# Performance work log

Measured on AMD Instinct MI355X. Metric: run time of the kernel, lower is better.

Reference implementation:

```python
import jax, jax.numpy as jnp
import numpy as np

EPS = 1e-6
DECAY = 0.9   # spike_decay
THR = 0.5     # spike_threshold
SBETA = 10.0  # surrogate beta
KW = 4        # depthwise short-conv kernel width (causal)


def _rms(x, w):
    return x * jax.lax.rsqrt(jnp.mean(x * x, axis=-1, keepdims=True) + EPS) * w


def setup_inputs() -> dict:
    B, T, D, H, dk, dv, r, dff = 2, 2048, 1024, 8, 64, 64, 64, 4096
    keys = iter(jax.random.split(jax.random.key(0), 24))
    def g(shape, s=0.02):
        return jax.random.normal(next(keys), shape, jnp.float32) * s
    return {
        'x': jax.random.normal(next(keys), (B, T, D), jnp.float32),
        'norm_in_w': jnp.ones((D,), jnp.float32),
        'conv_w': g((D, 1, KW), 0.3),
        'conv_b': jnp.zeros((D,), jnp.float32),
        'Wq': g((D, H * dk)),
        'Wk': g((D, H * dk)),
        'Wv': g((D, H * dv)),
        'Wo': g((H * dv, D)),
        'Wspike': g((D, H * dk), 0.1),  # larger init so LIF actually spikes
        'Wau': g((D, r)),
        'bau': jnp.zeros((r,), jnp.float32),
        'Wad': g((r, H * dk)),
        'bad': jnp.zeros((H * dk,), jnp.float32),
        'alpha_spike': jnp.zeros((1, H, dk), jnp.float32),
        'Wbeta': g((D, H)),
        'bbeta': jnp.zeros((H,), jnp.float32),
        'beta_spike': jnp.zeros((1, H, dk), jnp.float32),
        'head_norm_w': jnp.ones((H, dv), jnp.float32),
        'Wu1': g((D, r)),
        'bu1': jnp.zeros((r,), jnp.float32),
        'Wu2': g((r, D)),
        'bu2': jnp.zeros((D,), jnp.float32),
        'ff_norm_w': jnp.ones((D,), jnp.float32),
        'Wff1': g((D, dff)),
        'Wff3': g((D, dff)),
        'Wff2': g((dff, D)),
    }


def reference(x, norm_in_w, conv_w, conv_b, Wq, Wk, Wv, Wo, Wspike,
              Wau, bau, Wad, bad, alpha_spike, Wbeta, bbeta, beta_spike,
              head_norm_w, Wu1, bu1, Wu2, bu2, ff_norm_w, Wff1, Wff3, Wff2):
    B, T, D = x.shape
    H, dk = alpha_spike.shape[1], alpha_spike.shape[2]
    dv = head_norm_w.shape[1]

    # --- input norm + causal depthwise short conv + SiLU ---
    h = _rms(x, norm_in_w)
    hc = jnp.transpose(h, (0, 2, 1))                         # [B,D,T]
    conv = jax.lax.conv_general_dilated(
        hc, conv_w, window_strides=(1,), padding=[(KW - 1, 0)],
        dimension_numbers=('NCH', 'OIH', 'NCH'), feature_group_count=D)
    conv = conv + conv_b[None, :, None]
    h = jax.nn.silu(jnp.transpose(conv, (0, 2, 1)))          # [B,T,D]

    def heads(z, d):
        return z.reshape(B, T, H, d)

    q = heads(h @ Wq, dk)
    k = heads(h @ Wk, dk)
    v = heads(h @ Wv, dv)
    q = q / (jnp.linalg.norm(q, axis=-1, keepdims=True) + 1e-6)
    k = k / (jnp.linalg.norm(k, axis=-1, keepdims=True) + 1e-6)
    drive = heads(h @ Wspike, dk)                            # LIF drive [B,T,H,dk]
    alpha_base = heads(jax.nn.silu(h @ Wau + bau) @ Wad + bad, dk)
    beta_base = h @ Wbeta + bbeta                            # [B,T,H]

    asp = alpha_spike[0]                                     # [H,dk]
    bsp = beta_spike[0]                                      # [H,dk]

    def step(carry, ins):
        s, mem = carry                                       # s [B,H,dk,dv], mem [B,H,dk]
        qt, kt, vt, dt, at, bt = ins
        # LIF with surrogate-gradient spike (straight-through), soft reset
        mem = DECAY * mem + dt
        sg = jax.nn.sigmoid(SBETA * (mem - THR))
        hard = (mem > THR).astype(mem.dtype)
        spike = sg + jax.lax.stop_gradient(hard - sg)
        mem = mem - spike * THR
        # spiking-modulated gates
        alpha = jax.nn.sigmoid(at + asp * spike)             # [B,H,dk]
        beta = jax.nn.sigmoid(bt[..., None] + jnp.sum(spike * bsp, -1, keepdims=True))  # [B,H,1]
        active = (jnp.sum(jnp.abs(spike), -1, keepdims=True) > 0).astype(qt.dtype)      # [B,H,1]
        alpha = jnp.where(active > 0, alpha, jnp.ones_like(alpha))
        beta = beta * active
        # gated delta-rule fast-weight update
        s = s * alpha[..., None]
        pred = jnp.einsum('bhk,bhkv->bhv', kt, s)
        s = s + (beta * kt)[..., None] * (vt - pred)[:, :, None, :]
        out = jnp.einsum('bhk,bhkv->bhv', qt, s)
        return (s, mem), out

    s0 = jnp.zeros((B, H, dk, dv), x.dtype)
    m0 = jnp.zeros((B, H, dk), x.dtype)
    xs = (jnp.moveaxis(q, 1, 0), jnp.moveaxis(k, 1, 0), jnp.moveaxis(v, 1, 0),
          jnp.moveaxis(drive, 1, 0), jnp.moveaxis(alpha_base, 1, 0),
          jnp.moveaxis(beta_base, 1, 0))
    _, y = jax.lax.scan(step, (s0, m0), xs)                  # [T,B,H,dv]
    y = jnp.moveaxis(y, 0, 1)                                # [B,T,H,dv]

    # headwise RMS norm, merge heads
    y = y * jax.lax.rsqrt(jnp.mean(y * y, axis=-1, keepdims=True) + EPS) * head_norm_w
    y = y.reshape(B, T, H * dv)

    # gated output projection + residual
    gate = jax.nn.sigmoid(jax.nn.silu(x @ Wu1 + bu1) @ Wu2 + bu2)
    y = x + (y @ Wo) * gate

    # SwiGLU FFN + residual
    z = _rms(y, ff_norm_w)
    y = y + (jax.nn.silu(z @ Wff1) * (z @ Wff3)) @ Wff2
    return y
```

## Files before the change

kernel.cpp:

```cpp
#include <hip/hip_runtime.h>
#include <hip/hip_bf16.h>

#define BB 2
#define TT 2048
#define DD 1024
#define HH 8
#define HKk 512
#define BTt 4096
#define CC 16
#define NT 128
#define PREPSZ 4608

typedef unsigned short u16;
typedef __attribute__((ext_vector_type(8))) short bf16x8;
typedef __attribute__((ext_vector_type(4))) float f32x4;

__device__ __forceinline__ u16 f2bf(float v) {
  union { float f; unsigned u; } c; c.f = v;
  return (u16)((c.u + 0x7fffu + ((c.u >> 16) & 1u)) >> 16);
}
__device__ __forceinline__ float bf2f(u16 v) {
  union { unsigned u; float f; } c; c.u = ((unsigned)v) << 16; return c.f;
}
__device__ __forceinline__ float sigm(float x) { return 1.f / (1.f + expf(-x)); }

__device__ __forceinline__ void gld16(const u16* g, u16* l) {
  __builtin_amdgcn_global_load_lds((const __attribute__((address_space(1))) void*)g,
                                   (__attribute__((address_space(3))) void*)l, 16, 0, 0);
}

struct TransJobs {
  const float* src[8];
  u16* dst[8];
  int K[8], N[8], rs[8], ro[8], lognx[8];
  int off[8];
};
__global__ __launch_bounds__(256) void ktransB(TransJobs J) {
  __shared__ u16 t[32][33];
  int bid = blockIdx.x;
  int j = 0;
#pragma unroll
  for (int q = 1; q < 8; q++) j += (bid >= J.off[q]) ? 1 : 0;
  int local = bid - J.off[j];
  const float* src = J.src[j];
  u16* dst = J.dst[j];
  int K = J.K[j], N = J.N[j], rs = J.rs[j], ro = J.ro[j];
  int nxm = (1 << J.lognx[j]) - 1;
  int n0 = (local & nxm) * 32, k0 = (local >> J.lognx[j]) * 32;
  int tx = threadIdx.x & 31, ty0 = threadIdx.x >> 5;
#pragma unroll
  for (int i = 0; i < 32; i += 8)
    t[ty0 + i][tx] = f2bf(src[(size_t)(k0 + ty0 + i) * N + n0 + tx]);
  __syncthreads();
#pragma unroll
  for (int i = 0; i < 32; i += 8)
    dst[((size_t)(n0 + ty0 + i) * rs + ro) * K + k0 + tx] = t[tx][ty0 + i];
}

__global__ __launch_bounds__(256) void krms(const float* __restrict__ x,
                                            const float* __restrict__ w,
                                            void* __restrict__ out, int obf) {
  size_t row = blockIdx.x;
  __shared__ float red[4];
  float vals[4];
  float s = 0.f;
#pragma unroll
  for (int i = 0; i < 4; i++) {
    vals[i] = x[row * DD + threadIdx.x + i * 256];
    s += vals[i] * vals[i];
  }
#pragma unroll
  for (int off = 32; off; off >>= 1) s += __shfl_xor(s, off);
  if ((threadIdx.x & 63) == 0) red[threadIdx.x >> 6] = s;
  __syncthreads();
  float tot = red[0] + red[1] + red[2] + red[3];
  float sc = rsqrtf(tot * (1.f / DD) + 1e-6f);
#pragma unroll
  for (int i = 0; i < 4; i++) {
    size_t idx = row * DD + threadIdx.x + i * 256;
    float vv = vals[i] * sc * w[threadIdx.x + i * 256];
    if (obf) ((u16*)out)[idx] = f2bf(vv);
    else ((float*)out)[idx] = vv;
  }
}

__global__ __launch_bounds__(256) void kconv(const float* __restrict__ hin,
                                             const float* __restrict__ cw,
                                             const float* __restrict__ cb,
                                             u16* __restrict__ hout) {
  size_t i = (size_t)blockIdx.x * 256 + threadIdx.x;
  int d = (int)(i & 1023);
  int bt = (int)(i >> 10);
  int b = bt >> 11, t = bt & 2047;
  float acc = cb[d];
#pragma unroll
  for (int j = 0; j < 4; j++) {
    int tt = t - 3 + j;
    if (tt >= 0) acc += hin[(((size_t)(b * TT + tt)) << 10) + d] * cw[d * 4 + j];
  }
  hout[i] = f2bf(acc * sigm(acc));
}

__global__ __launch_bounds__(256) void kgemm(const void* __restrict__ A, int abf,
                                             const float* __restrict__ Bm,
                                             const float* __restrict__ bias,
                                             float* __restrict__ C,
                                             int M, int N, int K, int act) {
  __shared__ __align__(16) float As[16][64];
  __shared__ __align__(16) float Bs[16][64];
  int tid = threadIdx.x;
  int tx = tid & 15, ty = tid >> 4;
  int row0 = blockIdx.y * 64, col0 = blockIdx.x * 64;
  float acc[4][4] = {};
  for (int k0 = 0; k0 < K; k0 += 16) {
#pragma unroll
    for (int l = 0; l < 4; l++) {
      int e = tid * 4 + l;
      int m = e >> 4, kk = e & 15;
      int gr = row0 + m;
      size_t ai = (size_t)gr * K + k0 + kk;
      As[kk][m] = (gr < M) ? (abf ? bf2f(((const u16*)A)[ai]) : ((const float*)A)[ai]) : 0.f;
    }
#pragma unroll
    for (int l = 0; l < 4; l++) {
      int e = tid + l * 256;
      int kk = e >> 6, n = e & 63;
      int gc = col0 + n;
      Bs[kk][n] = (gc < N) ? Bm[(size_t)(k0 + kk) * N + gc] : 0.f;
    }
    __syncthreads();
#pragma unroll
    for (int kk = 0; kk < 16; kk++) {
      float4 av = *(const float4*)&As[kk][ty * 4];
      float4 bv = *(const float4*)&Bs[kk][tx * 4];
      float a[4] = {av.x, av.y, av.z, av.w};
      float b[4] = {bv.x, bv.y, bv.z, bv.w};
#pragma unroll
      for (int i = 0; i < 4; i++)
#pragma unroll
        for (int j = 0; j < 4; j++) acc[i][j] += a[i] * b[j];
    }
    __syncthreads();
  }
#pragma unroll
  for (int i = 0; i < 4; i++) {
    int r = row0 + ty * 4 + i;
    if (r >= M) continue;
#pragma unroll
    for (int j = 0; j < 4; j++) {
      int cc = col0 + tx * 4 + j;
      if (cc >= N) continue;
      float vv = acc[i][j];
      if (bias) vv += bias[cc];
      if (act == 1) vv = vv * sigm(vv);
      else if (act == 2) vv = sigm(vv);
      C[(size_t)r * N + cc] = vv;
    }
  }
}

struct SJobs {
  const void* A[3];
  const float* B[3];
  const float* bias[3];
  float* C[3];
  int N[3], act[3], abf[3];
};
__global__ __launch_bounds__(256) void kgemmS3(SJobs J) {
  __shared__ __align__(16) float As[32][17];
  __shared__ __align__(16) float Bs[32][64];
  int job = blockIdx.x >> 8;
  int row0 = (blockIdx.x & 255) << 4;
  const void* A = J.A[job];
  const float* Bm = J.B[job];
  int N = J.N[job], abf = J.abf[job], act = J.act[job];
  int tid = threadIdx.x;
  int tx = tid & 63;
  int ty = tid >> 6;
  float acc[4] = {};
  for (int k0 = 0; k0 < DD; k0 += 32) {
    __syncthreads();
#pragma unroll
    for (int l = 0; l < 2; l++) {
      int idx = tid * 2 + l;
      int k = idx & 31, m = idx >> 5;
      size_t ai = (size_t)(row0 + m) * DD + k0 + k;
      As[k][m] = abf ? bf2f(((const u16*)A)[ai]) : ((const float*)A)[ai];
    }
#pragma unroll
    for (int l = 0; l < 8; l++) {
      int idx = tid + l * 256;
      int n = idx & 63, k = idx >> 6;
      Bs[k][n] = (n < N) ? Bm[(size_t)(k0 + k) * N + n] : 0.f;
    }
    __syncthreads();
#pragma unroll
    for (int kk = 0; kk < 32; kk++) {
      float b = Bs[kk][tx];
#pragma unroll
      for (int i = 0; i < 4; i++) acc[i] += As[kk][ty * 4 + i] * b;
    }
  }
  if (tx < N) {
    float* C = J.C[job];
    const float* bias = J.bias[job];
#pragma unroll
    for (int i = 0; i < 4; i++) {
      float vv = acc[i] + bias[tx];
      if (act == 1) vv = vv * sigm(vv);
      C[(size_t)(row0 + ty * 4 + i) * N + tx] = vv;
    }
  }
}

template <int EPI>
__global__ __launch_bounds__(256) void kmfma(
    const u16* __restrict__ A, int lda, const u16* __restrict__ Bt,
    void* __restrict__ C, int ldc, int M, int N, int K,
    const float* __restrict__ g1f, const float* __restrict__ g2f,
    const float* __restrict__ f1) {
  __shared__ __align__(16) u16 As[128 * 64];
  __shared__ __align__(16) u16 Bs[128 * 64];
  int tid = threadIdx.x;
  int lane = tid & 63, wv = tid >> 6;
  int m0 = (wv & 1) * 64, n0 = (wv >> 1) * 64;
  int ml = lane & 15, kq = (lane >> 4) << 3;
  int nbx = gridDim.x;
  int flat = blockIdx.y * nbx + blockIdx.x;
  int nwg = nbx * gridDim.y;
  int work = (flat & 7) * (nwg >> 3) + (flat >> 3);
  int row0 = (work / nbx) * 128, col0 = (work % nbx) * 128;
  int lrow = lane >> 3;
  int lslot = (lane & 7) ^ lrow;

  f32x4 acc[4][4];
#pragma unroll
  for (int i = 0; i < 4; i++)
#pragma unroll
    for (int j = 0; j < 4; j++) acc[i][j] = (f32x4){0.f, 0.f, 0.f, 0.f};

  for (int k0 = 0; k0 < K; k0 += 64) {
    __syncthreads();
#pragma unroll
    for (int j = 0; j < 4; j++) {
      int r0 = j * 32 + wv * 8;
      gld16(&A[(size_t)(row0 + r0 + lrow) * lda + k0 + lslot * 8], &As[r0 * 64]);
      gld16(&Bt[(size_t)(col0 + r0 + lrow) * K + k0 + lslot * 8], &Bs[r0 * 64]);
    }
    __syncthreads();
#pragma unroll
    for (int kk = 0; kk < 64; kk += 32) {
      int sw = (((kk + kq) >> 3) ^ (ml & 7)) << 3;
      bf16x8 af[4], bfr[4];
#pragma unroll
      for (int i = 0; i < 4; i++)
        af[i] = *(const bf16x8*)&As[(m0 + i * 16 + ml) * 64 + sw];
#pragma unroll
      for (int j = 0; j < 4; j++)
        bfr[j] = *(const bf16x8*)&Bs[(n0 + j * 16 + ml) * 64 + sw];
#pragma unroll
      for (int i = 0; i < 4; i++)
#pragma unroll
        for (int j = 0; j < 4; j++)
          acc[i][j] = __builtin_amdgcn_mfma_f32_16x16x32_bf16(af[i], bfr[j], acc[i][j], 0, 0, 0);
    }
  }
  int rbase = row0 + m0 + ((lane >> 4) << 2);
  if (EPI == 4) {
    int donorm = (col0 + n0) < 1024;
#pragma unroll
    for (int i = 0; i < 4; i++) {
#pragma unroll
      for (int r = 0; r < 4; r++) {
        float s = 0.f;
#pragma unroll
        for (int j = 0; j < 4; j++) { float v = acc[i][j][r]; s += v * v; }
#pragma unroll
        for (int off = 1; off < 16; off <<= 1) s += __shfl_xor(s, off);
        float sc = donorm ? 1.f / (sqrtf(s) + 1e-6f) : 1.f;
        int gr = rbase + i * 16 + r;
#pragma unroll
        for (int j = 0; j < 4; j++) {
          int gc = col0 + n0 + j * 16 + ml;
          ((float*)C)[(size_t)gr * ldc + gc] = acc[i][j][r] * sc;
        }
      }
    }
    return;
  }
#pragma unroll
  for (int i = 0; i < 4; i++) {
#pragma unroll
    for (int j = 0; j < 4; j++) {
      int gc = col0 + n0 + j * 16 + ml;
#pragma unroll
      for (int r = 0; r < 4; r++) {
        int gr = rbase + i * 16 + r;
        float v = acc[i][j][r];
        if (EPI == 0) {
          ((float*)C)[(size_t)gr * ldc + gc] = v;
        } else if (EPI == 1) {
          float p = __shfl_xor(v, 1);
          float a0 = (lane & 1) ? p : v;
          float b0 = (lane & 1) ? v : p;
          float g = a0 * sigm(a0) * b0;
          if (!(lane & 1))
            ((u16*)C)[(size_t)gr * ldc + (gc >> 1)] = f2bf(g);
        } else if (EPI == 2) {
          size_t idx = (size_t)gr * ldc + gc;
          ((float*)C)[idx] = g1f[idx] + v * g2f[idx];
        } else {
          size_t idx = (size_t)gr * ldc + gc;
          ((float*)C)[idx] = f1[idx] + v;
        }
      }
    }
  }
}

__global__ __launch_bounds__(256) void kheadnorm(const float* __restrict__ y,
                                                 const float* __restrict__ hw,
                                                 u16* __restrict__ yo) {
  int lane = threadIdx.x & 63;
  size_t r = (size_t)blockIdx.x * 4 + (threadIdx.x >> 6);
  int h = (int)(r & 7);
  float vv = y[r * 64 + lane];
  float s = vv * vv;
#pragma unroll
  for (int off = 32; off; off >>= 1) s += __shfl_xor(s, off);
  yo[r * 64 + lane] = f2bf(vv * rsqrtf(s * (1.f / 64.f) + 1e-6f) * hw[h * 64 + lane]);
}

__global__ __launch_bounds__(64) void klifA(const float* __restrict__ dr, int drs,
                                            unsigned* __restrict__ masks) {
  int bh = blockIdx.x;
  int b = bh >> 3, h = bh & 7;
  int lane = threadIdx.x;
  float cur[32], nxt[32];
#pragma unroll
  for (int i = 0; i < 32; i++)
    cur[i] = dr[(size_t)(b * TT + i) * drs + h * 64 + lane];
  float mem = 0.f;
  for (int t0 = 0; t0 < TT; t0 += 32) {
    if (t0 + 32 < TT) {
#pragma unroll
      for (int i = 0; i < 32; i++)
        nxt[i] = dr[(size_t)(b * TT + t0 + 32 + i) * drs + h * 64 + lane];
    }
    unsigned m = 0;
#pragma unroll
    for (int i = 0; i < 32; i++) {
      mem = 0.9f * mem + cur[i];
      int s = (mem > 0.5f) ? 1 : 0;
      mem -= s ? 0.5f : 0.f;
      m |= ((unsigned)s) << i;
    }
    masks[((size_t)bh * 64 + (t0 >> 5)) * 64 + lane] = m;
#pragma unroll
    for (int i = 0; i < 32; i++) cur[i] = nxt[i];
  }
}

__global__ __launch_bounds__(64) void klifB(const unsigned* __restrict__ masks,
                                            const float* __restrict__ ab,
                                            const float* __restrict__ bb,
                                            const float* __restrict__ asp,
                                            const float* __restrict__ bsp,
                                            float* __restrict__ alpha,
                                            float* __restrict__ beta) {
  int blk = blockIdx.x;
  int bh = blk >> 4, tc = blk & 15;
  int b = bh >> 3, h = bh & 7;
  int lane = threadIdx.x;
  float aspk = asp[h * 64 + lane];
  float bspk = bsp[h * 64 + lane];
#pragma unroll
  for (int g = 0; g < 2; g++) {
    size_t row0 = (size_t)(b * TT) + tc * 128 + g * 64;
    unsigned m0 = masks[((size_t)bh * 64 + (tc * 4 + g * 2 + 0)) * 64 + lane];
    unsigned m1 = masks[((size_t)bh * 64 + (tc * 4 + g * 2 + 1)) * 64 + lane];
    float bbv = bb[(row0 + lane) * HH + h];
#pragma unroll
    for (int tt = 0; tt < 64; tt++) {
      unsigned mw = (tt < 32) ? m0 : m1;
      int s = (mw >> (tt & 31)) & 1;
      unsigned long long act = __ballot(s != 0);
      float sp = (float)s;
      float r2 = sp * bspk;
#pragma unroll
      for (int off = 32; off; off >>= 1) r2 += __shfl_xor(r2, off);
      float bbi = __shfl(bbv, tt);
      size_t rt = row0 + tt;
      float abv = ab[rt * HKk + h * 64 + lane];
      int active = (act != 0ull);
      alpha[rt * HKk + h * 64 + lane] = active ? sigm(abv + aspk * sp) : 1.f;
      if (lane == 0) beta[rt * HH + h] = active ? sigm(bbi + r2) : 0.f;
    }
  }
}

__global__ __launch_bounds__(64) void kprep(const float* __restrict__ X1,
                                            const float* __restrict__ alph,
                                            const float* __restrict__ beta,
                                            float* __restrict__ prep) {
  int blk = blockIdx.x;
  int bh = blk >> 7, T = blk & 127;
  int b = bh >> 3, h = bh & 7;
  int lane = threadIdx.x;
  size_t row0 = (size_t)(b * TT) + (size_t)T * CC;
  float* out = prep + (size_t)blk * PREPSZ;
  __shared__ float sKP[CC][68], sKiP[CC][68], sQP[CC][68];
  __shared__ float sBC[CC * CC], sG[CC * CC], sW[CC * CC], sBeta[CC];

  float Pt[CC], kv[CC], kh[CC];
  {
    float P = 1.f;
#pragma unroll
    for (int t = 0; t < CC; t++) {
      size_t rt = row0 + t;
      float a = alph[rt * HKk + h * 64 + lane];
      kv[t] = X1[rt * 2048 + h * 64 + 512 + lane];
      float qv = X1[rt * 2048 + h * 64 + lane];
      P *= a;
      Pt[t] = P;
      float qp = qv * P;
      sQP[t][lane] = qp;
      out[1024 + t * 64 + lane] = qp;
    }
    float PC = Pt[CC - 1];
#pragma unroll
    for (int t = 0; t < CC; t++) {
      float KiPv = kv[t] / Pt[t];
      sKP[t][lane] = kv[t] * Pt[t];
      sKiP[t][lane] = KiPv;
      kh[t] = PC * KiPv;
    }
    out[4096 + lane] = PC;
  }
  if (lane < CC) sBeta[lane] = beta[(row0 + lane) * HH + h];
  __syncthreads();
#pragma unroll
  for (int t = 0; t < CC; t++) out[t * 64 + lane] = sBeta[t] * kv[t] * Pt[t];

#pragma unroll
  for (int i = 0; i < 4; i++) {
    int p = lane + 64 * i;
    int t2 = p >> 4, s2 = p & 15;
    float ac = 0.f, ag = 0.f;
#pragma unroll
    for (int k = 0; k < 64; k++) {
      float kip = sKiP[s2][k];
      ac += sKP[t2][k] * kip;
      ag += sQP[t2][k] * kip;
    }
    sBC[p] = (t2 > s2) ? sBeta[t2] * ac : 0.f;
    sG[p] = (t2 >= s2) ? ag : 0.f;
    sW[p] = 0.f;
  }
  __syncthreads();
  if (lane < CC) sW[lane * CC + lane] = 1.f;
  __syncthreads();

  for (int t = 1; t < CC; t++) {
    if (lane < t) {
      float a = -sBC[t * CC + lane];
      for (int s = lane + 1; s < t; s++) a -= sBC[t * CC + s] * sW[s * CC + lane];
      sW[t * CC + lane] = a;
    }
    __syncthreads();
  }
#pragma unroll
  for (int i = 0; i < 4; i++) {
    int p = lane + 64 * i;
    int t2 = p >> 4, s2 = p & 15;
    float gw = 0.f;
    if (s2 <= t2)
      for (int m = s2; m <= t2; m++) gw += sG[t2 * CC + m] * sW[m * CC + s2];
    out[4160 + p] = gw;
  }
#pragma unroll
  for (int r = 0; r < CC; r++) {
    float acc = 0.f;
    for (int s = r; s < CC; s++) acc += kh[s] * sW[s * CC + r];
    out[2048 + r * 64 + lane] = acc;
  }
#pragma unroll
  for (int t = 0; t < CC; t++)
    out[3072 + t * 64 + lane] = sBeta[t] * X1[(row0 + t) * 2048 + h * 64 + 1024 + lane];
}

__global__ __launch_bounds__(64, 1) void kscan2(const float* __restrict__ prep,
                                                float* __restrict__ y) {
  int bid = blockIdx.x;
  int bh = bid & 15, vg = bid >> 4;
  int b = bh >> 3, h = bh & 7;
  int lane = threadIdx.x;
  int kp = lane & 15, vv = lane >> 4;
  const float* base = prep + (size_t)bh * NT * PREPSZ;

  float4 S = make_float4(0.f, 0.f, 0.f, 0.f);
  float4 k1A[16], q1A[16], k1B[16], q1B[16];
#pragma unroll
  for (int t = 0; t < CC; t++) {
    k1A[t] = *(const float4*)(base + t * 64 + kp * 4);
    q1A[t] = *(const float4*)(base + 1024 + t * 64 + kp * 4);
  }
  size_t yb = (size_t)(b * TT) * HKk + h * 64 + vg * 4 + vv;

#define TILEBODY(TI, K1, Q1, K1N, Q1N)                                          \
  do {                                                                          \
    const float* bp = base + (size_t)(TI)*PREPSZ;                               \
    int TN = ((TI) + 1 < NT) ? (TI) + 1 : NT - 1;                               \
    const float* np = base + (size_t)TN * PREPSZ;                               \
        \
    float4 kh2[16], gw[4], a15;                                                 \
    float bvs;                                                                  \
    _Pragma("unroll") for (int r = 0; r < CC; r++)                              \
        kh2[r] = *(const float4*)(bp + 2048 + r * 64 + kp * 4);                 \
    a15 = *(const float4*)(bp + 4096 + kp * 4);                                 \
    _Pragma("unroll") for (int i = 0; i < 4; i++)                               \
        gw[i] = *(const float4*)(bp + 4160 + kp * 16 + i * 4);                  \
    bvs = bp[3072 + kp * 64 + vg * 4 + vv];                                     \
                                \
    float bt[16], qb[16];                                                       \
    _Pragma("unroll") for (int t = 0; t < CC; t++) {                            \
      bt[t] = K1[t].x * S.x + K1[t].y * S.y + K1[t].z * S.z + K1[t].w * S.w;    \
      qb[t] = Q1[t].x * S.x + Q1[t].y * S.y + Q1[t].z * S.z + Q1[t].w * S.w;    \
    }                                                                           \
                                                \
    _Pragma("unroll") for (int t = 0; t < CC; t++) {                            \
      K1N[t] = *(const float4*)(np + t * 64 + kp * 4);                          \
      Q1N[t] = *(const float4*)(np + 1024 + t * 64 + kp * 4);                   \
    }                                                                           \
                                 \
    float b8[8], b4[4], b2[2], bS;                                              \
    _Pragma("unroll") for (int j = 0; j < 8; j++) {                             \
      float snd = (kp & 8) ? bt[j] : bt[j + 8];                                 \
      float rcv = __shfl_xor(snd, 8);                                           \
      b8[j] = ((kp & 8) ? bt[j + 8] : bt[j]) + rcv;                             \
    }                                                                           \
    _Pragma("unroll") for (int j = 0; j < 4; j++) {                             \
      float snd = (kp & 4) ? b8[j] : b8[j + 4];                                 \
      float rcv = __shfl_xor(snd, 4);                                           \
      b4[j] = ((kp & 4) ? b8[j + 4] : b8[j]) + rcv;                             \
    }                                                                           \
    _Pragma("unroll") for (int j = 0; j < 2; j++) {                             \
      float snd = (kp & 2) ? b4[j] : b4[j + 2];                                 \
      float rcv = __shfl_xor(snd, 2);                                           \
      b2[j] = ((kp & 2) ? b4[j + 2] : b4[j]) + rcv;                             \
    }                                                                           \
    {                                                                           \
      float snd = (kp & 1) ? b2[0] : b2[1];                                     \
      float rcv = __shfl_xor(snd, 1);                                           \
      bS = ((kp & 1) ? b2[1] : b2[0]) + rcv;                                    \
    }                                                                           \
    float uS = bvs - bS;                                                        \
                          \
    float u[16];                                                                \
    {                                                                           \
      float g = __shfl_xor(uS, 1);                                              \
      float a0 = (kp & 1) ? g : uS, a1 = (kp & 1) ? uS : g;                     \
      float g0 = __shfl_xor(a0, 2), g1 = __shfl_xor(a1, 2);                     \
      float c0 = (kp & 2) ? g0 : a0, c1 = (kp & 2) ? g1 : a1;                   \
      float c2 = (kp & 2) ? a0 : g0, c3 = (kp & 2) ? a1 : g1;                   \
      float h0 = __shfl_xor(c0, 4), h1 = __shfl_xor(c1, 4);                     \
      float h2 = __shfl_xor(c2, 4), h3 = __shfl_xor(c3, 4);                     \
      float d0 = (kp & 4) ? h0 : c0, d1 = (kp & 4) ? h1 : c1;                   \
      float d2 = (kp & 4) ? h2 : c2, d3 = (kp & 4) ? h3 : c3;                   \
      float d4 = (kp & 4) ? c0 : h0, d5 = (kp & 4) ? c1 : h1;                   \
      float d6 = (kp & 4) ? c2 : h2, d7 = (kp & 4) ? c3 : h3;                   \
      float e0 = __shfl_xor(d0, 8), e1 = __shfl_xor(d1, 8);                     \
      float e2 = __shfl_xor(d2, 8), e3 = __shfl_xor(d3, 8);                     \
      float e4 = __shfl_xor(d4, 8), e5 = __shfl_xor(d5, 8);                     \
      float e6 = __shfl_xor(d6, 8), e7 = __shfl_xor(d7, 8);                     \
      u[0] = (kp & 8) ? e0 : d0; u[1] = (kp & 8) ? e1 : d1;                     \
      u[2] = (kp & 8) ? e2 : d2; u[3] = (kp & 8) ? e3 : d3;                     \
      u[4] = (kp & 8) ? e4 : d4; u[5] = (kp & 8) ? e5 : d5;                     \
      u[6] = (kp & 8) ? e6 : d6; u[7] = (kp & 8) ? e7 : d7;                     \
      u[8] = (kp & 8) ? d0 : e0; u[9] = (kp & 8) ? d1 : e1;                     \
      u[10] = (kp & 8) ? d2 : e2; u[11] = (kp & 8) ? d3 : e3;                   \
      u[12] = (kp & 8) ? d4 : e4; u[13] = (kp & 8) ? d5 : e5;                   \
      u[14] = (kp & 8) ? d6 : e6; u[15] = (kp & 8) ? d7 : e7;                   \
    }                                                                           \
                                   \
    float p8[8], p4[4], p2[2], qsel;                                            \
    _Pragma("unroll") for (int j = 0; j < 8; j++) {                             \
      float snd = (kp & 8) ? qb[j] : qb[j + 8];                                 \
      float rcv = __shfl_xor(snd, 8);                                           \
      p8[j] = ((kp & 8) ? qb[j + 8] : qb[j]) + rcv;                             \
    }                                                                           \
    _Pragma("unroll") for (int j = 0; j < 4; j++) {                             \
      float snd = (kp & 4) ? p8[j] : p8[j + 4];                                 \
      float rcv = __shfl_xor(snd, 4);                                           \
      p4[j] = ((kp & 4) ? p8[j + 4] : p8[j]) + rcv;                             \
    }                                                                           \
    _Pragma("unroll") for (int j = 0; j < 2; j++) {                             \
      float snd = (kp & 2) ? p4[j] : p4[j + 2];                                 \
      float rcv = __shfl_xor(snd, 2);                                           \
      p2[j] = ((kp & 2) ? p4[j + 2] : p4[j]) + rcv;                             \
    }                                                                           \
    {                                                                           \
      float snd = (kp & 1) ? p2[0] : p2[1];                                     \
      float rcv = __shfl_xor(snd, 1);                                           \
      qsel = ((kp & 1) ? p2[1] : p2[0]) + rcv;                                  \
    }                                                                           \
                    \
    float o = qsel;                                                             \
    _Pragma("unroll") for (int i = 0; i < 4; i++)                               \
        o += gw[i].x * u[i * 4] + gw[i].y * u[i * 4 + 1] +                      \
             gw[i].z * u[i * 4 + 2] + gw[i].w * u[i * 4 + 3];                   \
    y[yb + (size_t)((TI)*CC + kp) * HKk] = o;                                   \
                          \
    S.x *= a15.x; S.y *= a15.y; S.z *= a15.z; S.w *= a15.w;                     \
    _Pragma("unroll") for (int r = 0; r < CC; r++) {                            \
      S.x += kh2[r].x * u[r]; S.y += kh2[r].y * u[r];                           \
      S.z += kh2[r].z * u[r]; S.w += kh2[r].w * u[r];                           \
    }                                                                           \
  } while (0)

  for (int T = 0; T < NT; T += 2) {
    TILEBODY(T, k1A, q1A, k1B, q1B);
    TILEBODY(T + 1, k1B, q1B, k1A, q1A);
  }
#undef TILEBODY
}

extern "C" void kernel_launch(void* const* d_in, const int* in_sizes, int n_in,
                              void* d_out, int out_size, void* d_ws, size_t ws_size,
                              hipStream_t stream) {
  const float *x = (const float*)d_in[0], *norm_in_w = (const float*)d_in[1],
              *conv_w = (const float*)d_in[2], *conv_b = (const float*)d_in[3],
              *Wq = (const float*)d_in[4], *Wk = (const float*)d_in[5],
              *Wv = (const float*)d_in[6], *Wo = (const float*)d_in[7],
              *Wspike = (const float*)d_in[8], *Wau = (const float*)d_in[9],
              *bau = (const float*)d_in[10], *Wad = (const float*)d_in[11],
              *bad_ = (const float*)d_in[12], *asp = (const float*)d_in[13],
              *Wbeta = (const float*)d_in[14], *bbeta = (const float*)d_in[15],
              *bsp = (const float*)d_in[16], *hnw = (const float*)d_in[17],
              *Wu1 = (const float*)d_in[18], *bu1 = (const float*)d_in[19],
              *Wu2 = (const float*)d_in[20], *bu2 = (const float*)d_in[21],
              *ffw = (const float*)d_in[22], *Wff1 = (const float*)d_in[23],
              *Wff3 = (const float*)d_in[24], *Wff2 = (const float*)d_in[25];
  (void)in_sizes; (void)n_in; (void)out_size; (void)ws_size;

  char* wsb = (char*)d_ws;
  size_t off = 0;
  auto alloc = [&](size_t bytes) {
    void* p = wsb + off;
    off += (bytes + 255) & ~(size_t)255;
    return p;
  };
  float* h    = (float*)alloc((size_t)BTt * DD * 4);
  u16*   hc   = (u16*)alloc((size_t)BTt * DD * 2);
  size_t qoff = off;
  float* X1   = (float*)alloc((size_t)BTt * 2048 * 4);
  float* ab   = (float*)alloc((size_t)BTt * HKk * 4);
  float* alph = (float*)alloc((size_t)BTt * HKk * 4);
  float* bb   = (float*)alloc((size_t)BTt * HH * 4);
  float* au   = (float*)alloc((size_t)BTt * 64 * 4);
  float* beta = (float*)alloc((size_t)BTt * HH * 4);
  float* u1   = (float*)alloc((size_t)BTt * 64 * 4);
  float* gate = (float*)alloc((size_t)BTt * DD * 4);
  float* yat  = (float*)alloc((size_t)BTt * HKk * 4);
  u16* yat_bf = (u16*)alloc((size_t)BTt * HKk * 2);
  u16* f_bf   = (u16*)(wsb + qoff);
  float* y2   = (float*)alloc((size_t)BTt * DD * 4);
  u16* z_bf   = (u16*)alloc((size_t)BTt * DD * 2);
  u16* WtX    = (u16*)alloc((size_t)2048 * 1024 * 2);
  u16* WtO    = (u16*)alloc((size_t)1024 * 512 * 2);
  u16* WtFF   = (u16*)alloc((size_t)8192 * 1024 * 2);
  u16* WtF2   = (u16*)alloc((size_t)1024 * 4096 * 2);
  float* prep = (float*)alloc((size_t)16 * NT * PREPSZ * 4);
  unsigned* masks = (unsigned*)alloc((size_t)16 * 64 * 64 * 4);

  {
    TransJobs J;
    J.src[0] = Wq;     J.dst[0] = WtX + (size_t)0 * 512 * 1024; J.K[0] = 1024; J.N[0] = 512;  J.rs[0] = 1; J.ro[0] = 0; J.lognx[0] = 4;
    J.src[1] = Wk;     J.dst[1] = WtX + (size_t)1 * 512 * 1024; J.K[1] = 1024; J.N[1] = 512;  J.rs[1] = 1; J.ro[1] = 0; J.lognx[1] = 4;
    J.src[2] = Wv;     J.dst[2] = WtX + (size_t)2 * 512 * 1024; J.K[2] = 1024; J.N[2] = 512;  J.rs[2] = 1; J.ro[2] = 0; J.lognx[2] = 4;
    J.src[3] = Wspike; J.dst[3] = WtX + (size_t)3 * 512 * 1024; J.K[3] = 1024; J.N[3] = 512;  J.rs[3] = 1; J.ro[3] = 0; J.lognx[3] = 4;
    J.src[4] = Wo;     J.dst[4] = WtO;                          J.K[4] = 512;  J.N[4] = 1024; J.rs[4] = 1; J.ro[4] = 0; J.lognx[4] = 5;
    J.src[5] = Wff1;   J.dst[5] = WtFF;                         J.K[5] = 1024; J.N[5] = 4096; J.rs[5] = 2; J.ro[5] = 0; J.lognx[5] = 7;
    J.src[6] = Wff3;   J.dst[6] = WtFF;                         J.K[6] = 1024; J.N[6] = 4096; J.rs[6] = 2; J.ro[6] = 1; J.lognx[6] = 7;
    J.src[7] = Wff2;   J.dst[7] = WtF2;                         J.K[7] = 4096; J.N[7] = 1024; J.rs[7] = 1; J.ro[7] = 0; J.lognx[7] = 5;
    J.off[0] = 0;    J.off[1] = 512;  J.off[2] = 1024; J.off[3] = 1536;
    J.off[4] = 2048; J.off[5] = 2560; J.off[6] = 6656; J.off[7] = 10752;
    ktransB<<<14848, 256, 0, stream>>>(J);
  }

  krms<<<BTt, 256, 0, stream>>>(x, norm_in_w, h, 0);
  kconv<<<BTt * DD / 256, 256, 0, stream>>>(h, conv_w, conv_b, hc);

  kmfma<4><<<dim3(16, 32), 256, 0, stream>>>(
      hc, 1024, WtX, X1, 2048, BTt, 2048, 1024, nullptr, nullptr, nullptr);

  {
    SJobs S;
    S.A[0] = hc; S.B[0] = Wau;   S.bias[0] = bau;   S.C[0] = au; S.N[0] = 64; S.act[0] = 1; S.abf[0] = 1;
    S.A[1] = hc; S.B[1] = Wbeta; S.bias[1] = bbeta; S.C[1] = bb; S.N[1] = 8;  S.act[1] = 0; S.abf[1] = 1;
    S.A[2] = x;  S.B[2] = Wu1;   S.bias[2] = bu1;   S.C[2] = u1; S.N[2] = 64; S.act[2] = 1; S.abf[2] = 0;
    kgemmS3<<<768, 256, 0, stream>>>(S);
  }
  kgemm<<<dim3(8, 64), 256, 0, stream>>>(au, 0, Wad, bad_, ab, BTt, HKk, 64, 0);

  klifA<<<BB * HH, 64, 0, stream>>>(X1 + 1536, 2048, masks);
  klifB<<<BB * HH * 16, 64, 0, stream>>>(masks, ab, bb, asp, bsp, alph, beta);
  kprep<<<16 * NT, 64, 0, stream>>>(X1, alph, beta, prep);
  kscan2<<<16 * 16, 64, 0, stream>>>(prep, yat);
  kheadnorm<<<BTt * HH / 4, 256, 0, stream>>>(yat, hnw, yat_bf);

  kgemm<<<dim3(16, 64), 256, 0, stream>>>(u1, 0, Wu2, bu2, gate, BTt, DD, 64, 2);

  kmfma<2><<<dim3(8, 32), 256, 0, stream>>>(
      yat_bf, 512, WtO, y2, 1024, BTt, 1024, 512, x, gate, nullptr);

  krms<<<BTt, 256, 0, stream>>>(y2, ffw, z_bf, 1);
  kmfma<1><<<dim3(64, 32), 256, 0, stream>>>(
      z_bf, 1024, WtFF, f_bf, 4096, BTt, 8192, 1024, nullptr, nullptr, nullptr);
  kmfma<3><<<dim3(8, 32), 256, 0, stream>>>(
      f_bf, 4096, WtF2, d_out, 1024, BTt, 1024, 4096, nullptr, nullptr, y2);
}
```

Baseline: 890.2 us.

## Split scan state across 32 key lanes to double block count in kscan2

The chunked delta-rule scan now gives each lane 2 key dimensions instead of 4, so a 64-lane block covers 2 value columns and the grid doubles to 512 blocks. Partial dot products get one extra cross-half shuffle reduction, and the output projection is split between the two 16-lane halves. The aim is to shorten the serial per-lane work and register footprint on the latency-bound recurrent scan, and to fill more CUs. The cost is extra shuffles and duplicated loads of per-tile data across more blocks.

```diff
diff --git a/kernel.cpp b/kernel.cpp
--- a/kernel.cpp
+++ b/kernel.cpp
@@ -495,126 +495,131 @@
   int bh = bid & 15, vg = bid >> 4;
   int b = bh >> 3, h = bh & 7;
   int lane = threadIdx.x;
-  int kp = lane & 15, vv = lane >> 4;
+  int kp = lane & 31;
+  int vv = lane >> 5;
+  int sg = kp >> 4, kpl = kp & 15;
   const float* base = prep + (size_t)bh * NT * PREPSZ;
 
-  float4 S = make_float4(0.f, 0.f, 0.f, 0.f);
-  float4 k1A[16], q1A[16], k1B[16], q1B[16];
+  float2 S = make_float2(0.f, 0.f);
+  float2 k1A[16], q1A[16], k1B[16], q1B[16];
 #pragma unroll
   for (int t = 0; t < CC; t++) {
-    k1A[t] = *(const float4*)(base + t * 64 + kp * 4);
-    q1A[t] = *(const float4*)(base + 1024 + t * 64 + kp * 4);
-  }
-  size_t yb = (size_t)(b * TT) * HKk + h * 64 + vg * 4 + vv;
+    k1A[t] = *(const float2*)(base + t * 64 + kp * 2);
+    q1A[t] = *(const float2*)(base + 1024 + t * 64 + kp * 2);
+  }
+  size_t yb = (size_t)(b * TT) * HKk + h * 64 + vg * 2 + vv;
 
 #define TILEBODY(TI, K1, Q1, K1N, Q1N)                                          \
   do {                                                                          \
     const float* bp = base + (size_t)(TI)*PREPSZ;                               \
     int TN = ((TI) + 1 < NT) ? (TI) + 1 : NT - 1;                               \
     const float* np = base + (size_t)TN * PREPSZ;                               \
-        \
-    float4 kh2[16], gw[4], a15;                                                 \
+                                          \
+    float2 kh2[16], a15;                                                        \
+    float4 gwa, gwb;                                                            \
     float bvs;                                                                  \
     _Pragma("unroll") for (int r = 0; r < CC; r++)                              \
-        kh2[r] = *(const float4*)(bp + 2048 + r * 64 + kp * 4);                 \
-    a15 = *(const float4*)(bp + 4096 + kp * 4);                                 \
-    _Pragma("unroll") for (int i = 0; i < 4; i++)                               \
-        gw[i] = *(const float4*)(bp + 4160 + kp * 16 + i * 4);                  \
-    bvs = bp[3072 + kp * 64 + vg * 4 + vv];                                     \
-                                \
+        kh2[r] = *(const float2*)(bp + 2048 + r * 64 + kp * 2);                 \
+    a15 = *(const float2*)(bp + 4096 + kp * 2);                                 \
+    gwa = *(const float4*)(bp + 4160 + kpl * 16 + sg * 8);                      \
+    gwb = *(const float4*)(bp + 4160 + kpl * 16 + sg * 8 + 4);                  \
+    bvs = bp[3072 + kpl * 64 + vg * 2 + vv];                                    \
+                                 \
     float bt[16], qb[16];                                                       \
     _Pragma("unroll") for (int t = 0; t < CC; t++) {                            \
-      bt[t] = K1[t].x * S.x + K1[t].y * S.y + K1[t].z * S.z + K1[t].w * S.w;    \
-      qb[t] = Q1[t].x * S.x + Q1[t].y * S.y + Q1[t].z * S.z + Q1[t].w * S.w;    \
+      bt[t] = K1[t].x * S.x + K1[t].y * S.y;                                    \
+      qb[t] = Q1[t].x * S.x + Q1[t].y * S.y;                                    \
     }                                                                           \
                                                 \
     _Pragma("unroll") for (int t = 0; t < CC; t++) {                            \
-      K1N[t] = *(const float4*)(np + t * 64 + kp * 4);                          \
-      Q1N[t] = *(const float4*)(np + 1024 + t * 64 + kp * 4);                   \
-    }                                                                           \
-                                 \
+      K1N[t] = *(const float2*)(np + t * 64 + kp * 2);                          \
+      Q1N[t] = *(const float2*)(np + 1024 + t * 64 + kp * 2);                   \
+    }                                                                           \
+          \
     float b8[8], b4[4], b2[2], bS;                                              \
     _Pragma("unroll") for (int j = 0; j < 8; j++) {                             \
-      float snd = (kp & 8) ? bt[j] : bt[j + 8];                                 \
+      float snd = (kpl & 8) ? bt[j] : bt[j + 8];                                \
       float rcv = __shfl_xor(snd, 8);                                           \
-      b8[j] = ((kp & 8) ? bt[j + 8] : bt[j]) + rcv;                             \
+      b8[j] = ((kpl & 8) ? bt[j + 8] : bt[j]) + rcv;                            \
     }                                                                           \
     _Pragma("unroll") for (int j = 0; j < 4; j++) {                             \
-      float snd = (kp & 4) ? b8[j] : b8[j + 4];                                 \
+      float snd = (kpl & 4) ? b8[j] : b8[j + 4];                                \
       float rcv = __shfl_xor(snd, 4);                                           \
-      b4[j] = ((kp & 4) ? b8[j + 4] : b8[j]) + rcv;                             \
+      b4[j] = ((kpl & 4) ? b8[j + 4] : b8[j]) + rcv;                            \
     }                                                                           \
     _Pragma("unroll") for (int j = 0; j < 2; j++) {                             \
-      float snd = (kp & 2) ? b4[j] : b4[j + 2];                                 \
+      float snd = (kpl & 2) ? b4[j] : b4[j + 2];                                \
       float rcv = __shfl_xor(snd, 2);                                           \
-      b2[j] = ((kp & 2) ? b4[j + 2] : b4[j]) + rcv;                             \
+      b2[j] = ((kpl & 2) ? b4[j + 2] : b4[j]) + rcv;                            \
     }                                                                           \
     {                                                                           \
-      float snd = (kp & 1) ? b2[0] : b2[1];                                     \
+      float snd = (kpl & 1) ? b2[0] : b2[1];                                    \
       float rcv = __shfl_xor(snd, 1);                                           \
-      bS = ((kp & 1) ? b2[1] : b2[0]) + rcv;                                    \
-    }                                                                           \
+      bS = ((kpl & 1) ? b2[1] : b2[0]) + rcv;                                   \
+    }                                                                           \
+    bS += __shfl_xor(bS, 16);                                                   \
     float uS = bvs - bS;                                                        \
-                          \
+    \
     float u[16];                                                                \
     {                                                                           \
       float g = __shfl_xor(uS, 1);                                              \
-      float a0 = (kp & 1) ? g : uS, a1 = (kp & 1) ? uS : g;                     \
+      float a0 = (kpl & 1) ? g : uS, a1 = (kpl & 1) ? uS : g;                   \
       float g0 = __shfl_xor(a0, 2), g1 = __shfl_xor(a1, 2);                     \
-      float c0 = (kp & 2) ? g0 : a0, c1 = (kp & 2) ? g1 : a1;                   \
-      float c2 = (kp & 2) ? a0 : g0, c3 = (kp & 2) ? a1 : g1;                   \
+      float c0 = (kpl & 2) ? g0 : a0, c1 = (kpl & 2) ? g1 : a1;                 \
+      float c2 = (kpl & 2) ? a0 : g0, c3 = (kpl & 2) ? a1 : g1;                 \
       float h0 = __shfl_xor(c0, 4), h1 = __shfl_xor(c1, 4);                     \
       float h2 = __shfl_xor(c2, 4), h3 = __shfl_xor(c3, 4);                     \
-      float d0 = (kp & 4) ? h0 : c0, d1 = (kp & 4) ? h1 : c1;                   \
-      float d2 = (kp & 4) ? h2 : c2, d3 = (kp & 4) ? h3 : c3;                   \
-      float d4 = (kp & 4) ? c0 : h0, d5 = (kp & 4) ? c1 : h1;                   \
-      float d6 = (kp & 4) ? c2 : h2, d7 = (kp & 4) ? c3 : h3;                   \
+      float d0 = (kpl & 4) ? h0 : c0, d1 = (kpl & 4) ? h1 : c1;                 \
+      float d2 = (kpl & 4) ? h2 : c2, d3 = (kpl & 4) ? h3 : c3;                 \
+      float d4 = (kpl & 4) ? c0 : h0, d5 = (kpl & 4) ? c1 : h1;                 \
+      float d6 = (kpl & 4) ? c2 : h2, d7 = (kpl & 4) ? c3 : h3;                 \
       float e0 = __shfl_xor(d0, 8), e1 = __shfl_xor(d1, 8);                     \
       float e2 = __shfl_xor(d2, 8), e3 = __shfl_xor(d3, 8);                     \
       float e4 = __shfl_xor(d4, 8), e5 = __shfl_xor(d5, 8);                     \
       float e6 = __shfl_xor(d6, 8), e7 = __shfl_xor(d7, 8);                     \
-      u[0] = (kp & 8) ? e0 : d0; u[1] = (kp & 8) ? e1 : d1;                     \
-      u[2] = (kp & 8) ? e2 : d2; u[3] = (kp & 8) ? e3 : d3;                     \
-      u[4] = (kp & 8) ? e4 : d4; u[5] = (kp & 8) ? e5 : d5;                     \
-      u[6] = (kp & 8) ? e6 : d6; u[7] = (kp & 8) ? e7 : d7;                     \
-      u[8] = (kp & 8) ? d0 : e0; u[9] = (kp & 8) ? d1 : e1;                     \
-      u[10] = (kp & 8) ? d2 : e2; u[11] = (kp & 8) ? d3 : e3;                   \
-      u[12] = (kp & 8) ? d4 : e4; u[13] = (kp & 8) ? d5 : e5;                   \
-      u[14] = (kp & 8) ? d6 : e6; u[15] = (kp & 8) ? d7 : e7;                   \
-    }                                                                           \
-                                   \
+      u[0] = (kpl & 8) ? e0 : d0; u[1] = (kpl & 8) ? e1 : d1;                   \
+      u[2] = (kpl & 8) ? e2 : d2; u[3] = (kpl & 8) ? e3 : d3;                   \
+      u[4] = (kpl & 8) ? e4 : d4; u[5] = (kpl & 8) ? e5 : d5;                   \
+      u[6] = (kpl & 8) ? e6 : d6; u[7] = (kpl & 8) ? e7 : d7;                   \
+      u[8] = (kpl & 8) ? d0 : e0; u[9] = (kpl & 8) ? d1 : e1;                   \
+      u[10] = (kpl & 8) ? d2 : e2; u[11] = (kpl & 8) ? d3 : e3;                 \
+      u[12] = (kpl & 8) ? d4 : e4; u[13] = (kpl & 8) ? d5 : e5;                 \
+      u[14] = (kpl & 8) ? d6 : e6; u[15] = (kpl & 8) ? d7 : e7;                 \
+    }                                                                           \
+           \
     float p8[8], p4[4], p2[2], qsel;                                            \
     _Pragma("unroll") for (int j = 0; j < 8; j++) {                             \
-      float snd = (kp & 8) ? qb[j] : qb[j + 8];                                 \
+      float snd = (kpl & 8) ? qb[j] : qb[j + 8];                                \
       float rcv = __shfl_xor(snd, 8);                                           \
-      p8[j] = ((kp & 8) ? qb[j + 8] : qb[j]) + rcv;                             \
+      p8[j] = ((kpl & 8) ? qb[j + 8] : qb[j]) + rcv;                            \
     }                                                                           \
     _Pragma("unroll") for (int j = 0; j < 4; j++) {                             \
-      float snd = (kp & 4) ? p8[j] : p8[j + 4];                                 \
+      float snd = (kpl & 4) ? p8[j] : p8[j + 4];                                \
       float rcv = __shfl_xor(snd, 4);                                           \
-      p4[j] = ((kp & 4) ? p8[j + 4] : p8[j]) + rcv;                             \
+      p4[j] = ((kpl & 4) ? p8[j + 4] : p8[j]) + rcv;                            \
     }                                                                           \
     _Pragma("unroll") for (int j = 0; j < 2; j++) {                             \
-      float snd = (kp & 2) ? p4[j] : p4[j + 2];                                 \
+      float snd = (kpl & 2) ? p4[j] : p4[j + 2];                                \
       float rcv = __shfl_xor(snd, 2);                                           \
-      p2[j] = ((kp & 2) ? p4[j + 2] : p4[j]) + rcv;                             \
+      p2[j] = ((kpl & 2) ? p4[j + 2] : p4[j]) + rcv;                            \
     }                                                                           \
     {                                                                           \
-      float snd = (kp & 1) ? p2[0] : p2[1];                                     \
+      float snd = (kpl & 1) ? p2[0] : p2[1];                                    \
       float rcv = __shfl_xor(snd, 1);                                           \
-      qsel = ((kp & 1) ? p2[1] : p2[0]) + rcv;                                  \
-    }                                                                           \
-                    \
-    float o = qsel;                                                             \
-    _Pragma("unroll") for (int i = 0; i < 4; i++)                               \
-        o += gw[i].x * u[i * 4] + gw[i].y * u[i * 4 + 1] +                      \
-             gw[i].z * u[i * 4 + 2] + gw[i].w * u[i * 4 + 3];                   \
-    y[yb + (size_t)((TI)*CC + kp) * HKk] = o;                                   \
+      qsel = ((kpl & 1) ? p2[1] : p2[0]) + rcv;                                 \
+    }                                                                           \
+       \
+    float ua[8];                                                                \
+    _Pragma("unroll") for (int i = 0; i < 8; i++) ua[i] = sg ? u[i + 8] : u[i]; \
+    float p = qsel + gwa.x * ua[0] + gwa.y * ua[1] + gwa.z * ua[2] +            \
+              gwa.w * ua[3] + gwb.x * ua[4] + gwb.y * ua[5] + gwb.z * ua[6] +   \
+              gwb.w * ua[7];                                                    \
+    p += __shfl_xor(p, 16);                                                     \
+    if (sg == 0) y[yb + (size_t)((TI)*CC + kpl) * HKk] = p;                     \
                           \
-    S.x *= a15.x; S.y *= a15.y; S.z *= a15.z; S.w *= a15.w;                     \
+    S.x *= a15.x; S.y *= a15.y;                                                 \
     _Pragma("unroll") for (int r = 0; r < CC; r++) {                            \
       S.x += kh2[r].x * u[r]; S.y += kh2[r].y * u[r];                           \
-      S.z += kh2[r].z * u[r]; S.w += kh2[r].w * u[r];                           \
     }                                                                           \
   } while (0)
 
@@ -706,7 +711,7 @@
   klifA<<<BB * HH, 64, 0, stream>>>(X1 + 1536, 2048, masks);
   klifB<<<BB * HH * 16, 64, 0, stream>>>(masks, ab, bb, asp, bsp, alph, beta);
   kprep<<<16 * NT, 64, 0, stream>>>(X1, alph, beta, prep);
-  kscan2<<<16 * 16, 64, 0, stream>>>(prep, yat);
+  kscan2<<<16 * 32, 64, 0, stream>>>(prep, yat);
   kheadnorm<<<BTt * HH / 4, 256, 0, stream>>>(yat, hnw, yat_bf);
 
   kgemm<<<dim3(16, 64), 256, 0, stream>>>(u1, 0, Wu2, bu2, gate, BTt, DD, 64, 2);
```

Measured after the change: 892.4 us. About the same (+0.2%).
